# Optimization experiments

Measured on AMD Instinct MI355X. Metric: run time of the kernel, lower is better.

The kernel has to match this reference:

```python
import jax, jax.numpy as jnp
import numpy as np

B, L, D, M, S = 1024, 50, 64, 100000, 2
NEG = float(-2**32 + 1)

def _ln(x):
    # F.layer_norm over last dim, no affine, eps=1e-8 (biased variance)
    mu = x.mean(-1, keepdims=True)
    var = ((x - mu) ** 2).mean(-1, keepdims=True)
    return (x - mu) / jnp.sqrt(var + 1e-8)

def setup_inputs():
    key = jax.random.key(0)
    ks = jax.random.split(key, 24)
    p = lambda i, shape: jax.random.normal(ks[i], shape, jnp.float32) * 0.05
    return {
        'user_items': jax.random.randint(ks[0], (B, L), 0, M + 1),
        'pos_items': jax.random.randint(ks[1], (B, L), 0, M + 1),
        'neg_items': jax.random.randint(ks[2], (B, L), 0, M + 1),
        'padding_mask': jnp.ones((B, L, 1), jnp.float32),
        'item_embedding': p(3, (M + 1, D)),
        'pos_embedding': p(4, (L, D)),
        'Q_sabs': p(5, (S, D, D)),
        'K_sabs': p(6, (S, D, D)),
        'V_sabs': p(7, (S, D, D)),
        'c1_w': p(8, (S, L, L)), 'c1_b': p(9, (S, L)),
        'c2_w': p(10, (S, L, L)), 'c2_b': p(11, (S, L)),
        'query_item': p(12, (1, 1, D)),
        'K_lba': p(13, (D, D)), 'V_lba': p(14, (D, D)),
        'l1_w': p(15, (1, 1)), 'l1_b': p(16, (1,)),
        'l2_w': p(17, (1, 1)), 'l2_b': p(18, (1,)),
        'gated_weight': p(19, (3 * D, 1)),
        'gated_bias': p(20, (1, 1)),
    }

def _forward(user_items, pos_items, neg_items, padding_mask, item_embedding,
             pos_embedding, Q_sabs, K_sabs, V_sabs, c1_w, c1_b, c2_w, c2_b,
             query_item, K_lba, V_lba, l1_w, l1_b, l2_w, l2_b,
             gated_weight, gated_bias):
    ie = item_embedding[user_items]                      # [B,L,D]
    inputs = ie + pos_embedding[None]                    # add positional (dropout = identity)
    inputs = inputs * padding_mask
    inputs = _ln(inputs)

    tril = jnp.tril(jnp.ones((L, L), inputs.dtype))
    key_mask = jnp.transpose(padding_mask, (0, 2, 1))    # [B,1,L]
    scale = D ** 0.5

    x = inputs
    for i in range(S):
        Qx = x @ Q_sabs[i]; Kx = x @ K_sabs[i]; Vx = x @ V_sabs[i]
        scores = jnp.einsum('bqd,bkd->bqk', Qx, Kx) / scale      # [B,L,L]
        scores = jnp.where(tril[None] == 0, NEG, scores)          # causal mask
        scores = jnp.where(key_mask == 0, NEG, scores)            # key padding mask
        scores = scores * padding_mask                            # query mask (NO softmax, as in source)
        att = jnp.einsum('bqk,bkd->bqd', scores, Vx) + x          # residual
        att = _ln(att)
        # Conv1d(L, L, 1) mixes across the sequence-position axis
        h = jax.nn.relu(jnp.einsum('ij,bjd->bid', c1_w[i], att) + c1_b[i][None, :, None])
        ff = jnp.einsum('ij,bjd->bid', c2_w[i], h) + c2_b[i][None, :, None] + att
        ff = ff * padding_mask
        x = _ln(ff)
    loc = x                                                       # [B,L,D]

    # location-based attention: single learned query over sequence
    Kx = inputs @ K_lba; Vx = inputs @ V_lba
    sc = jnp.einsum('qd,bld->bql', query_item[0], Kx)             # [B,1,L]
    sc = jnp.where(key_mask == 0, NEG, sc)
    sc = jax.nn.softmax(sc, axis=-1)
    glo = jnp.einsum('bql,bld->bqd', sc, Vx)                      # [B,1,D]
    glo = _ln(glo)
    h = jax.nn.relu(l1_w[0, 0] * glo + l1_b[0])                   # Conv1d(1,1,1) = scalar affine
    glo = l2_w[0, 0] * h + l2_b[0] + glo
    glo = _ln(glo)

    pos_e = item_embedding[pos_items]                             # [B,L,D]
    neg_e = item_embedding[neg_items]
    ms = jnp.concatenate([ie, ie], 0)                             # tile [2,1,1]
    y = jnp.tile(glo, (2, L, 1))                                  # [2B,L,D]
    mi = jnp.concatenate([pos_e, neg_e], 0)
    cat = jnp.concatenate([ms, y, mi], -1).reshape(-1, 3 * D)
    logits = (cat @ gated_weight + gated_bias).reshape(2 * B, L, 1)
    gating = jax.nn.sigmoid(jax.nn.sigmoid(logits))               # double sigmoid, as in source

    tl = jnp.concatenate([loc, loc], 0)
    tg = jnp.tile(glo, (2, 1, 1))
    out = tl * gating + tg * (1.0 - gating)
    out = out * jnp.concatenate([padding_mask, padding_mask], 0)
    out = _ln(out)
    op, on = out[:B], out[B:]
    return jnp.stack([jnp.sum(op * pos_e, -1), jnp.sum(on * neg_e, -1)], 0)  # [2,B,L]

def reference(user_items, pos_items, neg_items, padding_mask, item_embedding,
              pos_embedding, Q_sabs, K_sabs, V_sabs, c1_w, c1_b, c2_w, c2_b,
              query_item, K_lba, V_lba, l1_w, l1_b, l2_w, l2_b,
              gated_weight, gated_bias):
    return _forward(user_items, pos_items, neg_items, padding_mask, item_embedding,
                    pos_embedding, Q_sabs, K_sabs, V_sabs, c1_w, c1_b, c2_w, c2_b,
                    query_item, K_lba, V_lba, l1_w, l1_b, l2_w, l2_b,
                    gated_weight, gated_bias)
```

## Files before the change

kernel.cpp:

```cpp
#include <hip/hip_runtime.h>


#define NB 1024
#define LL 50
#define DD 64
#define LD 68
#define LDT 51
#define LDC 52
#define NR 7
#define NEGV (-4294967295.0f)

__device__ __forceinline__ float wsum(float v) {
#pragma unroll
  for (int m = 32; m >= 1; m >>= 1) v += __shfl_xor(v, m, 64);
  return v;
}
__device__ __forceinline__ float wmax(float v) {
#pragma unroll
  for (int m = 32; m >= 1; m >>= 1) v = fmaxf(v, __shfl_xor(v, m, 64));
  return v;
}
__device__ __forceinline__ float rowln(float v) {
  float m = wsum(v) * (1.f / 64.f);
  float df = v - m;
  float var = wsum(df * df) * (1.f / 64.f);
  return df / sqrtf(var + 1e-8f);
}
__device__ __forceinline__ float2 ld2(const float* p) {
  return *reinterpret_cast<const float2*>(p);
}
__device__ __forceinline__ float4 ld4(const float* p) {
  return *reinterpret_cast<const float4*>(p);
}

__global__ __launch_bounds__(512, 2) void fissa_kernel(
    const int* __restrict__ user_items, const int* __restrict__ pos_items,
    const int* __restrict__ neg_items, const float* __restrict__ pmask,
    const float* __restrict__ item_emb, const float* __restrict__ pos_emb,
    const float* __restrict__ Qs, const float* __restrict__ Ks,
    const float* __restrict__ Vs, const float* __restrict__ c1w,
    const float* __restrict__ c1b, const float* __restrict__ c2w,
    const float* __restrict__ c2b, const float* __restrict__ query,
    const float* __restrict__ Klba, const float* __restrict__ Vlba,
    const float* __restrict__ l1w, const float* __restrict__ l1b,
    const float* __restrict__ l2w, const float* __restrict__ l2b,
    const float* __restrict__ gw, const float* __restrict__ gb,
    float* __restrict__ out) {
  __shared__ __align__(16) float s_x[LL * LD];
  __shared__ __align__(16) float s_b[LL * LD];
  __shared__ __align__(16) float s_kt[DD * LDT + 64];
  __shared__ __align__(16) float s_c[LL * LDC];
  __shared__ __align__(16) float s_mask[64], s_qv[64], s_glo[64], s_sm[64],
      s_bias[64], s_gw[192], s_scal[2];

  const int b = blockIdx.x;
  const int tid = threadIdx.x;
  const int wv = tid >> 6, ln = tid & 63;

  int qrow[NR], qoff[NR], coff[NR];
  bool qok[NR];
#pragma unroll
  for (int r = 0; r < NR; ++r) {
    int q = wv + 8 * r;
    qok[r] = (q < LL);
    qrow[r] = qok[r] ? q : (LL - 1);
    qoff[r] = qrow[r] * LD;
    coff[r] = qrow[r] * LDC;
  }

  if (tid < 64) s_mask[tid] = (tid < LL) ? pmask[b * LL + tid] : 0.f;
  else if (tid < 128) s_qv[tid - 64] = query[tid - 64];
  else if (tid < 320) s_gw[tid - 128] = gw[tid - 128];

#pragma unroll
  for (int r = 0; r < NR; ++r) {
    int l = qrow[r];
    int u = user_items[b * LL + l];
    float mk = pmask[b * LL + l];
    float v = (item_emb[(size_t)u * DD + ln] + pos_emb[l * DD + ln]) * mk;
    float o = rowln(v);
    if (qok[r]) s_x[qoff[r] + ln] = o;
  }
  __syncthreads();

  {
    float akl[NR], avl[NR];
#pragma unroll
    for (int r = 0; r < NR; ++r) { akl[r] = 0.f; avl[r] = 0.f; }
    const float* Kc = Klba + ln;
    const float* Vc = Vlba + ln;
#pragma unroll 2
    for (int kc = 0; kc < DD; kc += 4) {
      float wk0 = Kc[kc * DD], wk1 = Kc[(kc + 1) * DD];
      float wk2 = Kc[(kc + 2) * DD], wk3 = Kc[(kc + 3) * DD];
      float wv0 = Vc[kc * DD], wv1 = Vc[(kc + 1) * DD];
      float wv2 = Vc[(kc + 2) * DD], wv3 = Vc[(kc + 3) * DD];
#pragma unroll
      for (int r = 0; r < NR; ++r) {
        float4 xv = ld4(&s_x[qoff[r] + kc]);
        akl[r] = fmaf(xv.x, wk0, fmaf(xv.y, wk1, fmaf(xv.z, wk2, fmaf(xv.w, wk3, akl[r]))));
        avl[r] = fmaf(xv.x, wv0, fmaf(xv.y, wv1, fmaf(xv.z, wv2, fmaf(xv.w, wv3, avl[r]))));
      }
    }
#pragma unroll
    for (int r = 0; r < NR; ++r)
      if (qok[r]) {
        s_kt[ln * LDT + qrow[r]] = akl[r];
        s_b[qoff[r] + ln] = avl[r];
      }
  }
  __syncthreads();

  if (wv == 0) {
    float sc = -INFINITY;
    {
      float acc = 0.f;
#pragma unroll 4
      for (int d = 0; d < DD; ++d) acc = fmaf(s_qv[d], s_kt[d * LDT + ln], acc);
      sc = acc;
      if (ln >= LL || s_mask[ln] == 0.f) sc = (ln < LL) ? NEGV : -INFINITY;
    }
    float mx = wmax(sc);
    float e = (ln < LL) ? expf(sc - mx) : 0.f;
    float den = wsum(e);
    if (ln < LL) s_sm[ln] = e / den;
    float acc = 0.f;
#pragma unroll 2
    for (int l = 0; l < LL; ++l) acc = fmaf(s_sm[l], s_b[l * LD + ln], acc);
    float g = rowln(acc);
    float h = fmaxf(l1w[0] * g + l1b[0], 0.f);
    float glo = rowln(l2w[0] * h + l2b[0] + g);
    s_glo[ln] = glo;
    float gs = wsum(glo * s_gw[64 + ln]);
    if (ln == 0) s_scal[0] = gs + gb[0];
  }
  __syncthreads();

#pragma unroll 1
  for (int i = 0; i < 2; ++i) {
    const float* Qc = Qs + i * DD * DD + ln;
    const float* Kc = Ks + i * DD * DD + ln;
    const float* Vc = Vs + i * DD * DD + ln;

    {
      float aq[NR], ak[NR];
#pragma unroll
      for (int r = 0; r < NR; ++r) { aq[r] = 0.f; ak[r] = 0.f; }
#pragma unroll 2
      for (int kc = 0; kc < DD; kc += 4) {
        float wq0 = Qc[kc * DD], wq1 = Qc[(kc + 1) * DD];
        float wq2 = Qc[(kc + 2) * DD], wq3 = Qc[(kc + 3) * DD];
        float wk0 = Kc[kc * DD], wk1 = Kc[(kc + 1) * DD];
        float wk2 = Kc[(kc + 2) * DD], wk3 = Kc[(kc + 3) * DD];
#pragma unroll
        for (int r = 0; r < NR; ++r) {
          float4 xv = ld4(&s_x[qoff[r] + kc]);
          aq[r] = fmaf(xv.x, wq0, fmaf(xv.y, wq1, fmaf(xv.z, wq2, fmaf(xv.w, wq3, aq[r]))));
          ak[r] = fmaf(xv.x, wk0, fmaf(xv.y, wk1, fmaf(xv.z, wk2, fmaf(xv.w, wk3, ak[r]))));
        }
      }
#pragma unroll
      for (int r = 0; r < NR; ++r)
        if (qok[r]) {
          s_b[qoff[r] + ln] = aq[r];
          s_kt[ln * LDT + qrow[r]] = ak[r];
        }
    }
    __syncthreads();

    {
      float sc[NR];
#pragma unroll
      for (int r = 0; r < NR; ++r) sc[r] = 0.f;
#pragma unroll 2
      for (int dc = 0; dc < DD; dc += 4) {
        float k0 = s_kt[dc * LDT + ln];
        float k1 = s_kt[(dc + 1) * LDT + ln];
        float k2 = s_kt[(dc + 2) * LDT + ln];
        float k3 = s_kt[(dc + 3) * LDT + ln];
#pragma unroll
        for (int r = 0; r < NR; ++r) {
          float4 qv = ld4(&s_b[qoff[r] + dc]);
          sc[r] = fmaf(qv.x, k0, fmaf(qv.y, k1, fmaf(qv.z, k2, fmaf(qv.w, k3, sc[r]))));
        }
      }
      if (ln < LL) {
        float mk = s_mask[ln];
#pragma unroll
        for (int r = 0; r < NR; ++r)
          if (qok[r]) {
            float v = sc[r] * 0.125f;
            if (ln > qrow[r]) v = NEGV;
            if (mk == 0.f) v = NEGV;
            v *= s_mask[qrow[r]];
            s_c[coff[r] + ln] = v;
          }
      }
    }
    __syncthreads();

    {
      float av[NR];
#pragma unroll
      for (int r = 0; r < NR; ++r) av[r] = 0.f;
#pragma unroll 2
      for (int kc = 0; kc < DD; kc += 4) {
        float wv0 = Vc[kc * DD], wv1 = Vc[(kc + 1) * DD];
        float wv2 = Vc[(kc + 2) * DD], wv3 = Vc[(kc + 3) * DD];
#pragma unroll
        for (int r = 0; r < NR; ++r) {
          float4 xv = ld4(&s_x[qoff[r] + kc]);
          av[r] = fmaf(xv.x, wv0, fmaf(xv.y, wv1, fmaf(xv.z, wv2, fmaf(xv.w, wv3, av[r]))));
        }
      }
#pragma unroll
      for (int r = 0; r < NR; ++r)
        if (qok[r]) s_b[qoff[r] + ln] = av[r];
    }
    __syncthreads();

    {
      float at[NR];
#pragma unroll
      for (int r = 0; r < NR; ++r) at[r] = s_x[qoff[r] + ln];
#pragma unroll 2
      for (int k = 0; k < 48; k += 4) {
        float v0 = s_b[k * LD + ln];
        float v1 = s_b[(k + 1) * LD + ln];
        float v2 = s_b[(k + 2) * LD + ln];
        float v3 = s_b[(k + 3) * LD + ln];
#pragma unroll
        for (int r = 0; r < NR; ++r) {
          float4 sv = ld4(&s_c[coff[r] + k]);
          at[r] = fmaf(sv.x, v0, fmaf(sv.y, v1, fmaf(sv.z, v2, fmaf(sv.w, v3, at[r]))));
        }
      }
      {
        float v0 = s_b[48 * LD + ln];
        float v1 = s_b[49 * LD + ln];
#pragma unroll
        for (int r = 0; r < NR; ++r) {
          float2 sv = ld2(&s_c[coff[r] + 48]);
          at[r] = fmaf(sv.x, v0, fmaf(sv.y, v1, at[r]));
        }
      }
#pragma unroll
      for (int r = 0; r < NR; ++r) {
        float o = rowln(at[r]);
        if (qok[r]) s_x[qoff[r] + ln] = o;
      }
    }
    __syncthreads();

    for (int e = tid; e < LL * LL; e += 512) {
      int q = e / LL;
      s_c[q * LDC + (e - q * LL)] = c1w[i * LL * LL + e];
    }
    if (tid < LL) s_bias[tid] = c1b[i * LL + tid];
    __syncthreads();

    {
      float hh[NR];
#pragma unroll
      for (int r = 0; r < NR; ++r) hh[r] = 0.f;
#pragma unroll 2
      for (int j = 0; j < 48; j += 4) {
        float x0 = s_x[j * LD + ln];
        float x1 = s_x[(j + 1) * LD + ln];
        float x2 = s_x[(j + 2) * LD + ln];
        float x3 = s_x[(j + 3) * LD + ln];
#pragma unroll
        for (int r = 0; r < NR; ++r) {
          float4 cv = ld4(&s_c[coff[r] + j]);
          hh[r] = fmaf(cv.x, x0, fmaf(cv.y, x1, fmaf(cv.z, x2, fmaf(cv.w, x3, hh[r]))));
        }
      }
      {
        float x0 = s_x[48 * LD + ln];
        float x1 = s_x[49 * LD + ln];
#pragma unroll
        for (int r = 0; r < NR; ++r) {
          float2 cv = ld2(&s_c[coff[r] + 48]);
          hh[r] = fmaf(cv.x, x0, fmaf(cv.y, x1, hh[r]));
        }
      }
#pragma unroll
      for (int r = 0; r < NR; ++r)
        if (qok[r]) s_b[qoff[r] + ln] = fmaxf(hh[r] + s_bias[qrow[r]], 0.f);
    }
    __syncthreads();

    for (int e = tid; e < LL * LL; e += 512) {
      int q = e / LL;
      s_c[q * LDC + (e - q * LL)] = c2w[i * LL * LL + e];
    }
    if (tid < LL) s_bias[tid] = c2b[i * LL + tid];
    __syncthreads();

    {
      float f0[NR];
#pragma unroll
      for (int r = 0; r < NR; ++r) f0[r] = s_x[qoff[r] + ln];
#pragma unroll 2
      for (int j = 0; j < 48; j += 4) {
        float h0 = s_b[j * LD + ln];
        float h1 = s_b[(j + 1) * LD + ln];
        float h2 = s_b[(j + 2) * LD + ln];
        float h3 = s_b[(j + 3) * LD + ln];
#pragma unroll
        for (int r = 0; r < NR; ++r) {
          float4 cv = ld4(&s_c[coff[r] + j]);
          f0[r] = fmaf(cv.x, h0, fmaf(cv.y, h1, fmaf(cv.z, h2, fmaf(cv.w, h3, f0[r]))));
        }
      }
      {
        float h0 = s_b[48 * LD + ln];
        float h1 = s_b[49 * LD + ln];
#pragma unroll
        for (int r = 0; r < NR; ++r) {
          float2 cv = ld2(&s_c[coff[r] + 48]);
          f0[r] = fmaf(cv.x, h0, fmaf(cv.y, h1, f0[r]));
        }
      }
#pragma unroll
      for (int r = 0; r < NR; ++r) {
        float v = (f0[r] + s_bias[qrow[r]]) * s_mask[qrow[r]];
        float o = rowln(v);
        if (qok[r]) s_x[qoff[r] + ln] = o;
      }
    }
    __syncthreads();
  }

  float g2c = s_scal[0];
  float gloc = s_glo[ln];
#pragma unroll 1
  for (int row = wv; row < 2 * LL; row += 8) {
    int sgn = row >= LL;
    int l = row - sgn * LL;
    int u = user_items[b * LL + l];
    int it = sgn ? neg_items[b * LL + l] : pos_items[b * LL + l];
    float ie_d = item_emb[(size_t)u * DD + ln];
    float mi_d = item_emb[(size_t)it * DD + ln];
    float logit = wsum(ie_d * s_gw[ln] + mi_d * s_gw[128 + ln]) + g2c;
    float sg = 1.f / (1.f + expf(-logit));
    float g = 1.f / (1.f + expf(-sg));
    float od = (s_x[l * LD + ln] * g + gloc * (1.f - g)) * s_mask[l];
    float o = rowln(od);
    float res = wsum(o * mi_d);
    if (ln == 0) out[(sgn * NB + b) * LL + l] = res;
  }
}

extern "C" void kernel_launch(void* const* d_in, const int* in_sizes, int n_in,
                              void* d_out, int out_size, void* d_ws, size_t ws_size,
                              hipStream_t stream) {
  const int* user_items = (const int*)d_in[0];
  const int* pos_items = (const int*)d_in[1];
  const int* neg_items = (const int*)d_in[2];
  const float* pmask = (const float*)d_in[3];
  const float* item_emb = (const float*)d_in[4];
  const float* pos_emb = (const float*)d_in[5];
  const float* Qs = (const float*)d_in[6];
  const float* Ks = (const float*)d_in[7];
  const float* Vs = (const float*)d_in[8];
  const float* c1w = (const float*)d_in[9];
  const float* c1b = (const float*)d_in[10];
  const float* c2w = (const float*)d_in[11];
  const float* c2b = (const float*)d_in[12];
  const float* query = (const float*)d_in[13];
  const float* Klba = (const float*)d_in[14];
  const float* Vlba = (const float*)d_in[15];
  const float* l1w = (const float*)d_in[16];
  const float* l1b = (const float*)d_in[17];
  const float* l2w = (const float*)d_in[18];
  const float* l2b = (const float*)d_in[19];
  const float* gw = (const float*)d_in[20];
  const float* gb = (const float*)d_in[21];
  float* out = (float*)d_out;

  fissa_kernel<<<dim3(NB), dim3(512), 0, stream>>>(
      user_items, pos_items, neg_items, pmask, item_emb, pos_emb, Qs, Ks, Vs,
      c1w, c1b, c2w, c2b, query, Klba, Vlba, l1w, l1b, l2w, l2b, gw, gb, out);
}
```

Measured before the change: 342.9 us.

## Fuse V projection into QK pass and prefetch conv weights to cut barriers

```diff
diff --git a/kernel.cpp b/kernel.cpp
--- a/kernel.cpp
+++ b/kernel.cpp
@@ -51,7 +51,7 @@
   __shared__ __align__(16) float s_kt[DD * LDT + 64];
   __shared__ __align__(16) float s_c[LL * LDC];
   __shared__ __align__(16) float s_mask[64], s_qv[64], s_glo[64], s_sm[64],
-      s_bias[64], s_gw[192], s_scal[2];
+      s_bias[64], s_bias2[64], s_gw[192], s_scal[2];
 
   const int b = blockIdx.x;
   const int tid = threadIdx.x;
@@ -142,21 +142,25 @@
     const float* Kc = Ks + i * DD * DD + ln;
     const float* Vc = Vs + i * DD * DD + ln;
 
+    float av[NR];
     {
       float aq[NR], ak[NR];
 #pragma unroll
-      for (int r = 0; r < NR; ++r) { aq[r] = 0.f; ak[r] = 0.f; }
+      for (int r = 0; r < NR; ++r) { aq[r] = 0.f; ak[r] = 0.f; av[r] = 0.f; }
 #pragma unroll 2
       for (int kc = 0; kc < DD; kc += 4) {
         float wq0 = Qc[kc * DD], wq1 = Qc[(kc + 1) * DD];
         float wq2 = Qc[(kc + 2) * DD], wq3 = Qc[(kc + 3) * DD];
         float wk0 = Kc[kc * DD], wk1 = Kc[(kc + 1) * DD];
         float wk2 = Kc[(kc + 2) * DD], wk3 = Kc[(kc + 3) * DD];
+        float wv0 = Vc[kc * DD], wv1 = Vc[(kc + 1) * DD];
+        float wv2 = Vc[(kc + 2) * DD], wv3 = Vc[(kc + 3) * DD];
 #pragma unroll
         for (int r = 0; r < NR; ++r) {
           float4 xv = ld4(&s_x[qoff[r] + kc]);
           aq[r] = fmaf(xv.x, wq0, fmaf(xv.y, wq1, fmaf(xv.z, wq2, fmaf(xv.w, wq3, aq[r]))));
           ak[r] = fmaf(xv.x, wk0, fmaf(xv.y, wk1, fmaf(xv.z, wk2, fmaf(xv.w, wk3, ak[r]))));
+          av[r] = fmaf(xv.x, wv0, fmaf(xv.y, wv1, fmaf(xv.z, wv2, fmaf(xv.w, wv3, av[r]))));
         }
       }
 #pragma unroll
@@ -199,23 +203,15 @@
     }
     __syncthreads();
 
-    {
-      float av[NR];
-#pragma unroll
-      for (int r = 0; r < NR; ++r) av[r] = 0.f;
-#pragma unroll 2
-      for (int kc = 0; kc < DD; kc += 4) {
-        float wv0 = Vc[kc * DD], wv1 = Vc[(kc + 1) * DD];
-        float wv2 = Vc[(kc + 2) * DD], wv3 = Vc[(kc + 3) * DD];
-#pragma unroll
-        for (int r = 0; r < NR; ++r) {
-          float4 xv = ld4(&s_x[qoff[r] + kc]);
-          av[r] = fmaf(xv.x, wv0, fmaf(xv.y, wv1, fmaf(xv.z, wv2, fmaf(xv.w, wv3, av[r]))));
-        }
-      }
-#pragma unroll
-      for (int r = 0; r < NR; ++r)
-        if (qok[r]) s_b[qoff[r] + ln] = av[r];
+#pragma unroll
+    for (int r = 0; r < NR; ++r)
+      if (qok[r]) {
+        s_b[qoff[r] + ln] = av[r];
+        if (ln < LL) s_kt[coff[r] + ln] = c1w[i * LL * LL + qrow[r] * LL + ln];
+      }
+    if (tid < LL) {
+      s_bias[tid] = c1b[i * LL + tid];
+      s_bias2[tid] = c2b[i * LL + tid];
     }
     __syncthreads();
 
@@ -252,14 +248,11 @@
     }
     __syncthreads();
 
-    for (int e = tid; e < LL * LL; e += 512) {
-      int q = e / LL;
-      s_c[q * LDC + (e - q * LL)] = c1w[i * LL * LL + e];
-    }
-    if (tid < LL) s_bias[tid] = c1b[i * LL + tid];
-    __syncthreads();
-
-    {
+    {
+#pragma unroll
+      for (int r = 0; r < NR; ++r)
+        if (qok[r] && ln < LL)
+          s_c[coff[r] + ln] = c2w[i * LL * LL + qrow[r] * LL + ln];
       float hh[NR];
 #pragma unroll
       for (int r = 0; r < NR; ++r) hh[r] = 0.f;
@@ -271,7 +264,7 @@
         float x3 = s_x[(j + 3) * LD + ln];
 #pragma unroll
         for (int r = 0; r < NR; ++r) {
-          float4 cv = ld4(&s_c[coff[r] + j]);
+          float4 cv = ld4(&s_kt[coff[r] + j]);
           hh[r] = fmaf(cv.x, x0, fmaf(cv.y, x1, fmaf(cv.z, x2, fmaf(cv.w, x3, hh[r]))));
         }
       }
@@ -280,7 +273,7 @@
         float x1 = s_x[49 * LD + ln];
 #pragma unroll
         for (int r = 0; r < NR; ++r) {
-          float2 cv = ld2(&s_c[coff[r] + 48]);
+          float2 cv = ld2(&s_kt[coff[r] + 48]);
           hh[r] = fmaf(cv.x, x0, fmaf(cv.y, x1, hh[r]));
         }
       }
@@ -288,13 +281,6 @@
       for (int r = 0; r < NR; ++r)
         if (qok[r]) s_b[qoff[r] + ln] = fmaxf(hh[r] + s_bias[qrow[r]], 0.f);
     }
-    __syncthreads();
-
-    for (int e = tid; e < LL * LL; e += 512) {
-      int q = e / LL;
-      s_c[q * LDC + (e - q * LL)] = c2w[i * LL * LL + e];
-    }
-    if (tid < LL) s_bias[tid] = c2b[i * LL + tid];
     __syncthreads();
 
     {
@@ -324,7 +310,7 @@
       }
 #pragma unroll
       for (int r = 0; r < NR; ++r) {
-        float v = (f0[r] + s_bias[qrow[r]]) * s_mask[qrow[r]];
+        float v = (f0[r] + s_bias2[qrow[r]]) * s_mask[qrow[r]];
         float o = rowln(v);
         if (qok[r]) s_x[qoff[r] + ln] = o;
       }
```

New measurement: 435.0 us. 1.27x slower.
